# Performance work log

Hardware: AMD Instinct MI355X
Metric: run time of the kernel (lower is better)

Reference implementation:

```python
import jax, jax.numpy as jnp
import numpy as np

N_EMBED = 1024
D_TOTAL = 512      # n_output_embed
N_GRID = 16        # n_output_size
H = 8              # n_heads
D_HEAD = D_TOTAL // H
HIDDEN = 4 * D_TOTAL
INIT_STD = 0.02


def setup_inputs() -> dict:
    key = jax.random.key(0)
    ks = jax.random.split(key, 12)
    s = INIT_STD
    return {
        "x": jax.random.normal(ks[0], (8, 4096, N_EMBED), dtype=jnp.float32),
        "mask": jnp.ones((8, 4096), dtype=bool),
        "W_kv": s * jax.random.normal(ks[1], (N_EMBED, 2 * D_TOTAL), dtype=jnp.float32),
        "b_kv": s * jax.random.normal(ks[2], (2 * D_TOTAL,), dtype=jnp.float32),
        "row_query": s * jax.random.normal(ks[3], (N_GRID, D_TOTAL // 2), dtype=jnp.float32),
        "col_query": s * jax.random.normal(ks[4], (N_GRID, D_TOTAL // 2), dtype=jnp.float32),
        "query_projection": s * jax.random.normal(ks[5], (D_TOTAL, D_TOTAL), dtype=jnp.float32),
        "W1": s * jax.random.normal(ks[6], (D_TOTAL, HIDDEN), dtype=jnp.float32),
        "b1": s * jax.random.normal(ks[7], (HIDDEN,), dtype=jnp.float32),
        "W2": s * jax.random.normal(ks[8], (HIDDEN, D_TOTAL), dtype=jnp.float32),
        "b2": s * jax.random.normal(ks[9], (D_TOTAL,), dtype=jnp.float32),
    }


def reference(x, mask, W_kv, b_kv, row_query, col_query, query_projection, W1, b1, W2, b2):
    b, s_len, _ = x.shape
    N, dt = N_GRID, D_TOTAL
    # Faithful to torch.einsum('ij,bnj->bnj', W, x): contract W over axis 0 only,
    # i.e. elementwise scale of x by W.sum(0). (Requires n_embed == 2*n_output_embed.)
    kv = x * jnp.sum(W_kv, axis=0) + b_kv                 # (b, s, 2*dt)
    k = kv[..., :dt].reshape(b, s_len, H, D_HEAD)
    v = kv[..., dt:].reshape(b, s_len, H, D_HEAD)
    # Grid queries: concat row/col halves, project.
    qg = jnp.concatenate([
        jnp.broadcast_to(row_query[:, None, :], (N, N, dt // 2)),
        jnp.broadcast_to(col_query[None, :, :], (N, N, dt // 2)),
    ], axis=2).reshape(N * N, dt)
    qg = (qg @ query_projection).reshape(N * N, H, D_HEAD)  # (q, h, d)
    # Scores over the sequence (no 1/sqrt(d) scaling in the original).
    scores = jnp.einsum('bshd,qhd->bshq', k, qg)           # (b, s, h, N*N)
    scores = jnp.where(mask[:, :, None, None], scores, -jnp.inf)
    att = jax.nn.softmax(scores, axis=1)                   # softmax over seq dim
    agg = jnp.einsum('bshd,bshq->bqhd', v, att).reshape(b, N * N, dt)
    # Residual MLP (dropout = 0, eval mode).
    mlp = jax.nn.gelu(agg @ W1 + b1) @ W2 + b2
    out = (agg + mlp).reshape(b, N, N, dt)
    return out
```

## Files before the change

### kernel.cpp

```cpp
#include <hip/hip_runtime.h>
#include <hip/hip_bf16.h>

typedef float f32x4 __attribute__((ext_vector_type(4)));
typedef __bf16 bf16x8 __attribute__((ext_vector_type(8)));
typedef unsigned short u16;
typedef u16 u16x8 __attribute__((ext_vector_type(8)));
typedef u16 u16x4 __attribute__((ext_vector_type(4)));

__device__ __forceinline__ u16 f2bf(float f) {
  unsigned int u = __builtin_bit_cast(unsigned int, f);
  u += 0x7fffu + ((u >> 16) & 1u);
  return (u16)(u >> 16);
}
__device__ __forceinline__ unsigned int pack2(float a, float b) {
  return (unsigned int)f2bf(a) | ((unsigned int)f2bf(b) << 16);
}
__device__ __forceinline__ f32x4 mfma_bf16(u16x8 a, u16x8 b, f32x4 c) {
  return __builtin_amdgcn_mfma_f32_16x16x32_bf16(
      __builtin_bit_cast(bf16x8, a), __builtin_bit_cast(bf16x8, b), c, 0, 0, 0);
}
__device__ __forceinline__ void gload16(const u16* g, u16* l) {
  __builtin_amdgcn_global_load_lds((const __attribute__((address_space(1))) void*)g,
                                   (__attribute__((address_space(3))) void*)l, 16, 0, 0);
}

__global__ void colsum1_kernel(const float* __restrict__ Wkv, float* __restrict__ wpart) {
  int bl = blockIdx.x, tid = threadIdx.x;
  float a[4] = {0.f, 0.f, 0.f, 0.f};
  for (int r = 0; r < 64; ++r) {
    int base = (bl * 64 + r) * 1024;
#pragma unroll
    for (int cc = 0; cc < 4; ++cc) a[cc] += Wkv[base + cc * 256 + tid];
  }
#pragma unroll
  for (int cc = 0; cc < 4; ++cc) wpart[bl * 1024 + cc * 256 + tid] = a[cc];
}
__global__ void colsum2_kernel(const float* __restrict__ wpart, float* __restrict__ wsum) {
  int c = blockIdx.x * 256 + threadIdx.x;
  float s = 0.f;
#pragma unroll
  for (int bl = 0; bl < 16; ++bl) s += wpart[bl * 1024 + c];
  wsum[c] = s;
}

__global__ void rowcol_kernel(const float* __restrict__ rq, const float* __restrict__ cq,
                              const float* __restrict__ P, float* __restrict__ AB) {
  int half = blockIdx.x >> 4, i = blockIdx.x & 15;
  int tid = threadIdx.x;
  const float* qsrc = half ? cq : rq;
  float a0 = 0.f, a1 = 0.f;
  for (int c = 0; c < 256; ++c) {
    float val = qsrc[i * 256 + c];
    int crow = half ? (256 + c) : c;
    a0 += val * P[crow * 512 + tid];
    a1 += val * P[crow * 512 + tid + 256];
  }
  AB[(half * 16 + i) * 512 + tid] = a0;
  AB[(half * 16 + i) * 512 + tid + 256] = a1;
}

__global__ __launch_bounds__(256) void transp_kernel(const float* __restrict__ src,
                                                     u16* __restrict__ dst, int R, int C) {
  __shared__ float t[64][65];
  int c0 = blockIdx.x * 64, r0 = blockIdx.y * 64;
  int tid = threadIdx.x;
  int col = tid & 63, rw = tid >> 6;
#pragma unroll
  for (int j = 0; j < 16; ++j) {
    int row = j * 4 + rw;
    t[row][col] = src[(size_t)(r0 + row) * C + c0 + col];
  }
  __syncthreads();
#pragma unroll
  for (int j = 0; j < 16; ++j) {
    int row = j * 4 + rw;
    dst[(size_t)(c0 + row) * R + r0 + col] = f2bf(t[col][row]);
  }
}

__global__ __launch_bounds__(256) void attn_partial_kernel(
    const float* __restrict__ x, const float* __restrict__ wsum,
    const float* __restrict__ bkv, const float* __restrict__ AB,
    float* __restrict__ part_o, float* __restrict__ part_d) {
  const int blk = blockIdx.x;
  const int b = blk >> 5;
  const int h = (blk >> 2) & 7;
  const int ch = blk & 3;
  const int tid = threadIdx.x;
  const int w = tid >> 6;
  const int l = tid & 63;
  const int l16 = l & 15;
  const int g = l >> 4;
  const int li = l & 31;
  const int hl = l >> 5;
  const int d2 = li << 1;

  __shared__ u16 Klds[64 * 72];
  __shared__ u16 Vt[64 * 72];
  __shared__ u16 Pt[256 * 72];

  const int hb = h * 64;
  const float2 wk = *(const float2*)&wsum[hb + d2];
  const float2 bk2 = *(const float2*)&bkv[hb + d2];
  const float2 wv = *(const float2*)&wsum[512 + hb + d2];
  const float2 bv2 = *(const float2*)&bkv[512 + hb + d2];

  u16x8 qf[4][2];
#pragma unroll
  for (int nt = 0; nt < 4; ++nt) {
#pragma unroll
    for (int kk = 0; kk < 2; ++kk) {
      int qq = w * 64 + nt * 16 + l16;
      int col = hb + kk * 32 + g * 8;
      float4 ra = *(const float4*)&AB[(qq >> 4) * 512 + col];
      float4 rb = *(const float4*)&AB[(qq >> 4) * 512 + col + 4];
      float4 ca = *(const float4*)&AB[(16 + (qq & 15)) * 512 + col];
      float4 cb = *(const float4*)&AB[(16 + (qq & 15)) * 512 + col + 4];
      u16x8 f;
      f[0] = f2bf(ra.x + ca.x); f[1] = f2bf(ra.y + ca.y);
      f[2] = f2bf(ra.z + ca.z); f[3] = f2bf(ra.w + ca.w);
      f[4] = f2bf(rb.x + cb.x); f[5] = f2bf(rb.y + cb.y);
      f[6] = f2bf(rb.z + cb.z); f[7] = f2bf(rb.w + cb.w);
      qf[nt][kk] = f;
    }
  }

  f32x4 acc[4][4];
#pragma unroll
  for (int m = 0; m < 4; ++m)
#pragma unroll
    for (int nt = 0; nt < 4; ++nt) acc[m][nt] = (f32x4){0.f, 0.f, 0.f, 0.f};
  float dsum[4] = {0.f, 0.f, 0.f, 0.f};

  const int sbase = b * 4096 + ch * 1024;

  for (int t = 0; t < 16; ++t) {
    if (t) __syncthreads();
    const int s0 = sbase + t * 64;
#pragma unroll
    for (int j = 0; j < 8; ++j) {
      int row = w * 16 + j * 2 + hl;
      const float* xr = &x[(s0 + row) * 1024 + hb + d2];
      float2 xk = *(const float2*)xr;
      float2 xv = *(const float2*)(xr + 512);
      float k0 = fmaf(xk.x, wk.x, bk2.x);
      float k1 = fmaf(xk.y, wk.y, bk2.y);
      float v0 = fmaf(xv.x, wv.x, bv2.x);
      float v1 = fmaf(xv.y, wv.y, bv2.y);
      *(unsigned int*)&Klds[row * 72 + d2] = pack2(k0, k1);
      Vt[d2 * 72 + row] = f2bf(v0);
      Vt[(d2 + 1) * 72 + row] = f2bf(v1);
    }
    __syncthreads();

#pragma unroll
    for (int mss = 0; mss < 4; ++mss) {
      u16x8 ka0 = *(const u16x8*)&Klds[(mss * 16 + l16) * 72 + g * 8];
      u16x8 ka1 = *(const u16x8*)&Klds[(mss * 16 + l16) * 72 + 32 + g * 8];
#pragma unroll
      for (int nt = 0; nt < 4; ++nt) {
        f32x4 s = (f32x4){0.f, 0.f, 0.f, 0.f};
        s = mfma_bf16(ka0, qf[nt][0], s);
        s = mfma_bf16(ka1, qf[nt][1], s);
        float p0 = __expf(s[0]);
        float p1 = __expf(s[1]);
        float p2 = __expf(s[2]);
        float p3 = __expf(s[3]);
        dsum[nt] += (p0 + p1) + (p2 + p3);
        u16x4 pk;
        pk[0] = f2bf(p0); pk[1] = f2bf(p1); pk[2] = f2bf(p2); pk[3] = f2bf(p3);
        int qq = w * 64 + nt * 16 + l16;
        int ssb = mss * 16 + g * 4;
        *(u16x4*)&Pt[qq * 72 + ssb] = pk;
      }
    }
    asm volatile("" ::: "memory");

#pragma unroll
    for (int kk = 0; kk < 2; ++kk) {
      u16x8 pa[4], vb[4];
#pragma unroll
      for (int m = 0; m < 4; ++m)
        pa[m] = *(const u16x8*)&Pt[(w * 64 + m * 16 + l16) * 72 + kk * 32 + g * 8];
#pragma unroll
      for (int nt = 0; nt < 4; ++nt)
        vb[nt] = *(const u16x8*)&Vt[(nt * 16 + l16) * 72 + kk * 32 + g * 8];
#pragma unroll
      for (int m = 0; m < 4; ++m)
#pragma unroll
        for (int nt = 0; nt < 4; ++nt)
          acc[m][nt] = mfma_bf16(pa[m], vb[nt], acc[m][nt]);
    }
  }

  const int bhch = (b * 8 + h) * 4 + ch;
#pragma unroll
  for (int nt = 0; nt < 4; ++nt) {
    float dv = dsum[nt];
    dv += __shfl_xor(dv, 16);
    dv += __shfl_xor(dv, 32);
    if (l < 16) part_d[bhch * 256 + w * 64 + nt * 16 + l] = dv;
  }
#pragma unroll
  for (int m = 0; m < 4; ++m)
#pragma unroll
    for (int nt = 0; nt < 4; ++nt)
#pragma unroll
      for (int r = 0; r < 4; ++r) {
        int qq = w * 64 + m * 16 + g * 4 + r;
        int d = nt * 16 + l16;
        part_o[(bhch * 256 + qq) * 64 + d] = acc[m][nt][r];
      }
}

__global__ void combine_kernel(const float* __restrict__ part_o,
                               const float* __restrict__ part_d,
                               float* __restrict__ agg, u16* __restrict__ aggb) {
  int idx = blockIdx.x * 256 + threadIdx.x;
  int c = idx & 511;
  int q = (idx >> 9) & 255;
  int b = idx >> 17;
  int h = c >> 6, d = c & 63;
  int bh = b * 8 + h;
  float o = 0.f, den = 0.f;
#pragma unroll
  for (int ch = 0; ch < 4; ++ch) {
    o += part_o[((bh * 4 + ch) * 256 + q) * 64 + d];
    den += part_d[(bh * 4 + ch) * 256 + q];
  }
  float r = o / den;
  agg[idx] = r;
  aggb[idx] = f2bf(r);
}

__device__ __forceinline__ void gemm_main(const u16* __restrict__ A, const u16* __restrict__ B,
                                          int K, int m0, int n0, int k0, int nit,
                                          u16* Alds, u16* Blds, f32x4 (&acc)[4][2],
                                          int w, int l) {
  const int wm = w >> 1, wn = w & 1;
  const int l16 = l & 15, g = l >> 4;
  const int lr = l >> 3, lc = (l & 7) * 8;
  for (int it = 0; it < nit; ++it) {
    int kb = k0 + it * 64;
    if (it) __syncthreads();
#pragma unroll
    for (int i = 0; i < 4; ++i) {
      int r = i * 32 + w * 8 + lr;
      gload16(&A[(size_t)(m0 + r) * K + kb + lc], &Alds[(i * 32 + w * 8) * 64]);
    }
#pragma unroll
    for (int i = 0; i < 2; ++i) {
      int r = i * 32 + w * 8 + lr;
      gload16(&B[(size_t)(n0 + r) * K + kb + lc], &Blds[(i * 32 + w * 8) * 64]);
    }
    __syncthreads();
#pragma unroll
    for (int kk = 0; kk < 2; ++kk) {
      u16x8 af[4], bf[2];
#pragma unroll
      for (int mi = 0; mi < 4; ++mi)
        af[mi] = *(const u16x8*)&Alds[(wm * 64 + mi * 16 + l16) * 64 + kk * 32 + g * 8];
#pragma unroll
      for (int ni = 0; ni < 2; ++ni)
        bf[ni] = *(const u16x8*)&Blds[(wn * 32 + ni * 16 + l16) * 64 + kk * 32 + g * 8];
#pragma unroll
      for (int mi = 0; mi < 4; ++mi)
#pragma unroll
        for (int ni = 0; ni < 2; ++ni)
          acc[mi][ni] = mfma_bf16(af[mi], bf[ni], acc[mi][ni]);
    }
  }
}

__global__ __launch_bounds__(256) void gemm1_kernel(
    const u16* __restrict__ aggb, const u16* __restrict__ W1t,
    const float* __restrict__ b1, u16* __restrict__ h1) {
  __shared__ u16 Alds[128 * 64];
  __shared__ u16 Blds[64 * 64];
  const int m0 = blockIdx.x * 128, n0 = blockIdx.y * 64;
  const int tid = threadIdx.x, w = tid >> 6, l = tid & 63;
  f32x4 acc[4][2];
#pragma unroll
  for (int mi = 0; mi < 4; ++mi)
#pragma unroll
    for (int ni = 0; ni < 2; ++ni) acc[mi][ni] = (f32x4){0.f, 0.f, 0.f, 0.f};
  gemm_main(aggb, W1t, 512, m0, n0, 0, 8, Alds, Blds, acc, w, l);
  const int wm = w >> 1, wn = w & 1, l16 = l & 15, g = l >> 4;
#pragma unroll
  for (int ni = 0; ni < 2; ++ni) {
    int n = n0 + wn * 32 + ni * 16 + l16;
    float bias = b1[n];
#pragma unroll
    for (int mi = 0; mi < 4; ++mi)
#pragma unroll
      for (int r = 0; r < 4; ++r) {
        int m = m0 + wm * 64 + mi * 16 + g * 4 + r;
        float u = acc[mi][ni][r] + bias;
        float t = tanhf(0.7978845608028654f * (u + 0.044715f * u * u * u));
        h1[(size_t)m * 2048 + n] = f2bf(0.5f * u * (1.f + t));
      }
  }
}

__global__ __launch_bounds__(256) void gemm2_kernel(
    const u16* __restrict__ h1, const u16* __restrict__ W2t,
    float* __restrict__ part2) {
  __shared__ u16 Alds[128 * 64];
  __shared__ u16 Blds[64 * 64];
  const int m0 = blockIdx.x * 128, n0 = blockIdx.y * 64;
  const int split = blockIdx.z;
  const int tid = threadIdx.x, w = tid >> 6, l = tid & 63;
  f32x4 acc[4][2];
#pragma unroll
  for (int mi = 0; mi < 4; ++mi)
#pragma unroll
    for (int ni = 0; ni < 2; ++ni) acc[mi][ni] = (f32x4){0.f, 0.f, 0.f, 0.f};
  gemm_main(h1, W2t, 2048, m0, n0, split * 512, 8, Alds, Blds, acc, w, l);
  const int wm = w >> 1, wn = w & 1, l16 = l & 15, g = l >> 4;
  float* pbase = part2 + (size_t)split * 2048 * 512;
#pragma unroll
  for (int ni = 0; ni < 2; ++ni) {
    int n = n0 + wn * 32 + ni * 16 + l16;
#pragma unroll
    for (int mi = 0; mi < 4; ++mi)
#pragma unroll
      for (int r = 0; r < 4; ++r) {
        int m = m0 + wm * 64 + mi * 16 + g * 4 + r;
        pbase[(size_t)m * 512 + n] = acc[mi][ni][r];
      }
  }
}

__global__ void combine2_kernel(const float* __restrict__ part2, const float* __restrict__ b2,
                                const float* __restrict__ agg, float* __restrict__ out) {
  int idx = blockIdx.x * 256 + threadIdx.x;
  int e = idx * 4;
  int n = e & 511;
  float4 s = *(const float4*)&part2[e];
  float4 s1 = *(const float4*)&part2[1048576 + e];
  float4 s2 = *(const float4*)&part2[2097152 + e];
  float4 s3 = *(const float4*)&part2[3145728 + e];
  float4 bb = *(const float4*)&b2[n];
  float4 aa = *(const float4*)&agg[e];
  float4 o;
  o.x = s.x + s1.x + s2.x + s3.x + bb.x + aa.x;
  o.y = s.y + s1.y + s2.y + s3.y + bb.y + aa.y;
  o.z = s.z + s1.z + s2.z + s3.z + bb.z + aa.z;
  o.w = s.w + s1.w + s2.w + s3.w + bb.w + aa.w;
  *(float4*)&out[e] = o;
}

extern "C" void kernel_launch(void* const* d_in, const int* in_sizes, int n_in,
                              void* d_out, int out_size, void* d_ws, size_t ws_size,
                              hipStream_t stream) {
  const float* x   = (const float*)d_in[0];
  const float* Wkv = (const float*)d_in[2];
  const float* bkv = (const float*)d_in[3];
  const float* rq  = (const float*)d_in[4];
  const float* cq  = (const float*)d_in[5];
  const float* qp  = (const float*)d_in[6];
  const float* W1  = (const float*)d_in[7];
  const float* b1  = (const float*)d_in[8];
  const float* W2  = (const float*)d_in[9];
  const float* b2  = (const float*)d_in[10];
  float* out = (float*)d_out;

  float* ws = (float*)d_ws;
  float* wsum   = ws;
  float* wpart  = ws + 1024;
  float* AB     = ws + 17408;
  float* agg    = ws + 33792;
  float* part_o = ws + 1082368;
  float* part_d = ws + 5276672;
  u16*   h1     = (u16*)(ws + 5342208);
  u16*   W1t    = (u16*)(ws + 7439360);
  u16*   W2t    = (u16*)(ws + 7963648);
  u16*   aggb   = (u16*)(ws + 8487936);
  float* part2  = part_o;

  colsum1_kernel<<<16, 256, 0, stream>>>(Wkv, wpart);
  colsum2_kernel<<<4, 256, 0, stream>>>(wpart, wsum);
  rowcol_kernel<<<32, 256, 0, stream>>>(rq, cq, qp, AB);
  transp_kernel<<<dim3(32, 8), 256, 0, stream>>>(W1, W1t, 512, 2048);
  transp_kernel<<<dim3(8, 32), 256, 0, stream>>>(W2, W2t, 2048, 512);
  attn_partial_kernel<<<256, 256, 0, stream>>>(x, wsum, bkv, AB, part_o, part_d);
  combine_kernel<<<4096, 256, 0, stream>>>(part_o, part_d, agg, aggb);
  gemm1_kernel<<<dim3(16, 32), 256, 0, stream>>>(aggb, W1t, b1, h1);
  gemm2_kernel<<<dim3(16, 8, 4), 256, 0, stream>>>(h1, W2t, part2);
  combine2_kernel<<<1024, 256, 0, stream>>>(part2, b2, agg, out);
}
```

Measured before the change: 119.1 us.

## Split attention into more sequence chunks with larger blocks and bf16 partial outputs

The attention partial kernel now runs 512 blocks of 512 threads. Each block covers 512 sequence rows instead of 1024, and each of its 8 waves handles 32 queries instead of 64. This is meant to fill more of the GPU's compute units and raise per-CU wave occupancy. V loads are rewritten so each lane reads one column across two rows and packs them into Vt with a single 32-bit store instead of two 16-bit scattered stores. Partial outputs are written in bf16 to hold down the traffic of the doubled chunk count, at the cost of extra precision loss and a combine kernel that now reads 8 partials per output.

Measured after the change: 112.7 us. 1.06x faster.

```diff
diff --git a/kernel.cpp b/kernel.cpp
--- a/kernel.cpp
+++ b/kernel.cpp
@@ -11,6 +11,9 @@
   unsigned int u = __builtin_bit_cast(unsigned int, f);
   u += 0x7fffu + ((u >> 16) & 1u);
   return (u16)(u >> 16);
+}
+__device__ __forceinline__ float bf2f(u16 v) {
+  return __builtin_bit_cast(float, (unsigned int)v << 16);
 }
 __device__ __forceinline__ unsigned int pack2(float a, float b) {
   return (unsigned int)f2bf(a) | ((unsigned int)f2bf(b) << 16);
@@ -78,14 +81,14 @@
   }
 }
 
-__global__ __launch_bounds__(256) void attn_partial_kernel(
+__global__ __launch_bounds__(512, 4) void attn_partial_kernel(
     const float* __restrict__ x, const float* __restrict__ wsum,
     const float* __restrict__ bkv, const float* __restrict__ AB,
-    float* __restrict__ part_o, float* __restrict__ part_d) {
+    u16* __restrict__ part_o, float* __restrict__ part_d) {
   const int blk = blockIdx.x;
-  const int b = blk >> 5;
-  const int h = (blk >> 2) & 7;
-  const int ch = blk & 3;
+  const int b = blk >> 6;
+  const int h = (blk >> 3) & 7;
+  const int ch = blk & 7;
   const int tid = threadIdx.x;
   const int w = tid >> 6;
   const int l = tid & 63;
@@ -102,15 +105,15 @@
   const int hb = h * 64;
   const float2 wk = *(const float2*)&wsum[hb + d2];
   const float2 bk2 = *(const float2*)&bkv[hb + d2];
-  const float2 wv = *(const float2*)&wsum[512 + hb + d2];
-  const float2 bv2 = *(const float2*)&bkv[512 + hb + d2];
-
-  u16x8 qf[4][2];
-#pragma unroll
-  for (int nt = 0; nt < 4; ++nt) {
+  const float wvl = wsum[512 + hb + l];
+  const float bvl = bkv[512 + hb + l];
+
+  u16x8 qf[2][2];
+#pragma unroll
+  for (int nt = 0; nt < 2; ++nt) {
 #pragma unroll
     for (int kk = 0; kk < 2; ++kk) {
-      int qq = w * 64 + nt * 16 + l16;
+      int qq = w * 32 + nt * 16 + l16;
       int col = hb + kk * 32 + g * 8;
       float4 ra = *(const float4*)&AB[(qq >> 4) * 512 + col];
       float4 rb = *(const float4*)&AB[(qq >> 4) * 512 + col + 4];
@@ -125,31 +128,32 @@
     }
   }
 
-  f32x4 acc[4][4];
-#pragma unroll
-  for (int m = 0; m < 4; ++m)
+  f32x4 acc[2][4];
+#pragma unroll
+  for (int m = 0; m < 2; ++m)
 #pragma unroll
     for (int nt = 0; nt < 4; ++nt) acc[m][nt] = (f32x4){0.f, 0.f, 0.f, 0.f};
-  float dsum[4] = {0.f, 0.f, 0.f, 0.f};
-
-  const int sbase = b * 4096 + ch * 1024;
-
-  for (int t = 0; t < 16; ++t) {
+  float dsum[2] = {0.f, 0.f};
+
+  const int sbase = b * 4096 + ch * 512;
+
+  for (int t = 0; t < 8; ++t) {
     if (t) __syncthreads();
     const int s0 = sbase + t * 64;
 #pragma unroll
-    for (int j = 0; j < 8; ++j) {
-      int row = w * 16 + j * 2 + hl;
-      const float* xr = &x[(s0 + row) * 1024 + hb + d2];
-      float2 xk = *(const float2*)xr;
-      float2 xv = *(const float2*)(xr + 512);
-      float k0 = fmaf(xk.x, wk.x, bk2.x);
-      float k1 = fmaf(xk.y, wk.y, bk2.y);
-      float v0 = fmaf(xv.x, wv.x, bv2.x);
-      float v1 = fmaf(xv.y, wv.y, bv2.y);
-      *(unsigned int*)&Klds[row * 72 + d2] = pack2(k0, k1);
-      Vt[d2 * 72 + row] = f2bf(v0);
-      Vt[(d2 + 1) * 72 + row] = f2bf(v1);
+    for (int j = 0; j < 4; ++j) {
+      int row = w * 8 + j * 2 + hl;
+      float2 xk = *(const float2*)&x[(size_t)(s0 + row) * 1024 + hb + d2];
+      *(unsigned int*)&Klds[row * 72 + d2] =
+          pack2(fmaf(xk.x, wk.x, bk2.x), fmaf(xk.y, wk.y, bk2.y));
+    }
+#pragma unroll
+    for (int jp = 0; jp < 4; ++jp) {
+      int r = w * 8 + jp * 2;
+      float va = x[(size_t)(s0 + r) * 1024 + 512 + hb + l];
+      float vb_ = x[(size_t)(s0 + r + 1) * 1024 + 512 + hb + l];
+      *(unsigned int*)&Vt[l * 72 + r] =
+          pack2(fmaf(va, wvl, bvl), fmaf(vb_, wvl, bvl));
     }
     __syncthreads();
 
@@ -158,7 +162,7 @@
       u16x8 ka0 = *(const u16x8*)&Klds[(mss * 16 + l16) * 72 + g * 8];
       u16x8 ka1 = *(const u16x8*)&Klds[(mss * 16 + l16) * 72 + 32 + g * 8];
 #pragma unroll
-      for (int nt = 0; nt < 4; ++nt) {
+      for (int nt = 0; nt < 2; ++nt) {
         f32x4 s = (f32x4){0.f, 0.f, 0.f, 0.f};
         s = mfma_bf16(ka0, qf[nt][0], s);
         s = mfma_bf16(ka1, qf[nt][1], s);
@@ -169,51 +173,49 @@
         dsum[nt] += (p0 + p1) + (p2 + p3);
         u16x4 pk;
         pk[0] = f2bf(p0); pk[1] = f2bf(p1); pk[2] = f2bf(p2); pk[3] = f2bf(p3);
-        int qq = w * 64 + nt * 16 + l16;
-        int ssb = mss * 16 + g * 4;
-        *(u16x4*)&Pt[qq * 72 + ssb] = pk;
+        *(u16x4*)&Pt[(w * 32 + nt * 16 + l16) * 72 + mss * 16 + g * 4] = pk;
       }
     }
     asm volatile("" ::: "memory");
 
 #pragma unroll
     for (int kk = 0; kk < 2; ++kk) {
-      u16x8 pa[4], vb[4];
-#pragma unroll
-      for (int m = 0; m < 4; ++m)
-        pa[m] = *(const u16x8*)&Pt[(w * 64 + m * 16 + l16) * 72 + kk * 32 + g * 8];
+      u16x8 pa[2], vb[4];
+#pragma unroll
+      for (int m = 0; m < 2; ++m)
+        pa[m] = *(const u16x8*)&Pt[(w * 32 + m * 16 + l16) * 72 + kk * 32 + g * 8];
 #pragma unroll
       for (int nt = 0; nt < 4; ++nt)
         vb[nt] = *(const u16x8*)&Vt[(nt * 16 + l16) * 72 + kk * 32 + g * 8];
 #pragma unroll
-      for (int m = 0; m < 4; ++m)
+      for (int m = 0; m < 2; ++m)
 #pragma unroll
         for (int nt = 0; nt < 4; ++nt)
           acc[m][nt] = mfma_bf16(pa[m], vb[nt], acc[m][nt]);
     }
   }
 
-  const int bhch = (b * 8 + h) * 4 + ch;
-#pragma unroll
-  for (int nt = 0; nt < 4; ++nt) {
+  const int bhch = (b * 8 + h) * 8 + ch;
+#pragma unroll
+  for (int nt = 0; nt < 2; ++nt) {
     float dv = dsum[nt];
     dv += __shfl_xor(dv, 16);
     dv += __shfl_xor(dv, 32);
-    if (l < 16) part_d[bhch * 256 + w * 64 + nt * 16 + l] = dv;
-  }
-#pragma unroll
-  for (int m = 0; m < 4; ++m)
+    if (l < 16) part_d[bhch * 256 + w * 32 + nt * 16 + l] = dv;
+  }
+#pragma unroll
+  for (int m = 0; m < 2; ++m)
 #pragma unroll
     for (int nt = 0; nt < 4; ++nt)
 #pragma unroll
       for (int r = 0; r < 4; ++r) {
-        int qq = w * 64 + m * 16 + g * 4 + r;
+        int qq = w * 32 + m * 16 + g * 4 + r;
         int d = nt * 16 + l16;
-        part_o[(bhch * 256 + qq) * 64 + d] = acc[m][nt][r];
+        part_o[((size_t)bhch * 256 + qq) * 64 + d] = f2bf(acc[m][nt][r]);
       }
 }
 
-__global__ void combine_kernel(const float* __restrict__ part_o,
+__global__ void combine_kernel(const u16* __restrict__ part_o,
                                const float* __restrict__ part_d,
                                float* __restrict__ agg, u16* __restrict__ aggb) {
   int idx = blockIdx.x * 256 + threadIdx.x;
@@ -224,9 +226,9 @@
   int bh = b * 8 + h;
   float o = 0.f, den = 0.f;
 #pragma unroll
-  for (int ch = 0; ch < 4; ++ch) {
-    o += part_o[((bh * 4 + ch) * 256 + q) * 64 + d];
-    den += part_d[(bh * 4 + ch) * 256 + q];
+  for (int ch = 0; ch < 8; ++ch) {
+    o += bf2f(part_o[((size_t)(bh * 8 + ch) * 256 + q) * 64 + d]);
+    den += part_d[(bh * 8 + ch) * 256 + q];
   }
   float r = o / den;
   agg[idx] = r;
@@ -370,20 +372,20 @@
   float* wpart  = ws + 1024;
   float* AB     = ws + 17408;
   float* agg    = ws + 33792;
-  float* part_o = ws + 1082368;
+  u16*   part_o = (u16*)(ws + 1082368);
+  float* part2  = ws + 1082368;
   float* part_d = ws + 5276672;
-  u16*   h1     = (u16*)(ws + 5342208);
-  u16*   W1t    = (u16*)(ws + 7439360);
-  u16*   W2t    = (u16*)(ws + 7963648);
-  u16*   aggb   = (u16*)(ws + 8487936);
-  float* part2  = part_o;
+  u16*   h1     = (u16*)(ws + 5407744);
+  u16*   W1t    = (u16*)(ws + 7504896);
+  u16*   W2t    = (u16*)(ws + 8029184);
+  u16*   aggb   = (u16*)(ws + 8553472);
 
   colsum1_kernel<<<16, 256, 0, stream>>>(Wkv, wpart);
   colsum2_kernel<<<4, 256, 0, stream>>>(wpart, wsum);
   rowcol_kernel<<<32, 256, 0, stream>>>(rq, cq, qp, AB);
   transp_kernel<<<dim3(32, 8), 256, 0, stream>>>(W1, W1t, 512, 2048);
   transp_kernel<<<dim3(8, 32), 256, 0, stream>>>(W2, W2t, 2048, 512);
-  attn_partial_kernel<<<256, 256, 0, stream>>>(x, wsum, bkv, AB, part_o, part_d);
+  attn_partial_kernel<<<512, 512, 0, stream>>>(x, wsum, bkv, AB, part_o, part_d);
   combine_kernel<<<4096, 256, 0, stream>>>(part_o, part_d, agg, aggb);
   gemm1_kernel<<<dim3(16, 32), 256, 0, stream>>>(aggb, W1t, b1, h1);
   gemm2_kernel<<<dim3(16, 8, 4), 256, 0, stream>>>(h1, W2t, part2);
```
